# Performance work log

Measured on AMD Instinct MI355X. Metric: run time of the kernel, lower is better.

## Reference

```python
import jax, jax.numpy as jnp
import numpy as np

N = 8000      # nodes
E = 64000     # edges
F = 2560      # in_channels
H = 8         # heads
C = 320       # out_channels per head
G = 16        # graphs in batch
SLOPE = 0.2   # GATv2 default negative_slope


def setup_inputs() -> dict:
    key = jax.random.key(0)
    ks = jax.random.split(key, 20)
    inp = {
        'x': jax.random.normal(ks[0], (N, F), jnp.float32),
        'edge_index': jax.random.randint(ks[1], (2, E), 0, N, dtype=jnp.int64),
        'edge_attr': jax.random.normal(ks[2], (E, 1), jnp.float32),
        'batch': jnp.sort(jax.random.randint(ks[3], (N,), 0, G, dtype=jnp.int64)),
    }
    s_in = 1.0 / np.sqrt(F).astype(np.float32)
    s_att = 1.0 / np.sqrt(C).astype(np.float32)
    k = 4
    for layer in (1, 2):
        inp[f'Wl{layer}'] = jax.random.normal(ks[k + 0], (F, H * C), jnp.float32) * s_in
        inp[f'bl{layer}'] = jnp.zeros((H * C,), jnp.float32)
        inp[f'Wr{layer}'] = jax.random.normal(ks[k + 1], (F, H * C), jnp.float32) * s_in
        inp[f'br{layer}'] = jnp.zeros((H * C,), jnp.float32)
        inp[f'We{layer}'] = jax.random.normal(ks[k + 2], (1, H * C), jnp.float32)
        inp[f'att{layer}'] = jax.random.normal(ks[k + 3], (H, C), jnp.float32) * s_att
        inp[f'bias{layer}'] = jnp.zeros((H * C,), jnp.float32)
        k += 4
    return inp


def gatv2_layer(x, src, dst, edge_attr, Wl, bl, Wr, br, We, att, bias):
    # x: [N,F] -> out: [N, H*C]
    xl = (x @ Wl + bl).reshape(N, H, C)   # source transform (aggregated)
    xr = (x @ Wr + br).reshape(N, H, C)   # target transform
    ee = (edge_attr @ We).reshape(E, H, C)
    m = jax.nn.leaky_relu(xl[src] + xr[dst] + ee, SLOPE)  # [E,H,C]
    score = jnp.einsum('ehc,hc->eh', m, att)               # [E,H]
    # segment softmax over incoming edges of each target node
    smax = jax.ops.segment_max(score, dst, num_segments=N)  # [N,H]
    ex = jnp.exp(score - smax[dst])
    denom = jax.ops.segment_sum(ex, dst, num_segments=N)    # [N,H]
    alpha = ex / denom[dst]                                  # [E,H]
    out = jax.ops.segment_sum(xl[src] * alpha[:, :, None], dst, num_segments=N)
    return out.reshape(N, H * C) + bias


def reference(x, edge_index, edge_attr, batch,
              Wl1, bl1, Wr1, br1, We1, att1, bias1,
              Wl2, bl2, Wr2, br2, We2, att2, bias2):
    src, dst = edge_index[0], edge_index[1]
    h = gatv2_layer(x, src, dst, edge_attr, Wl1, bl1, Wr1, br1, We1, att1, bias1)
    # dropout is identity in eval mode
    h = gatv2_layer(h, src, dst, edge_attr, Wl2, bl2, Wr2, br2, We2, att2, bias2)
    # global mean pool over graphs
    sums = jax.ops.segment_sum(h, batch, num_segments=G)                 # [G, H*C]
    cnt = jax.ops.segment_sum(jnp.ones((N, 1), h.dtype), batch, num_segments=G)
    return sums / jnp.maximum(cnt, 1.0)
```

## Files before the change

kernel.cpp:

```cpp
#include <hip/hip_runtime.h>

typedef unsigned short u16;
typedef _Float16 f16;
typedef _Float16 f16x8 __attribute__((ext_vector_type(8)));
typedef float f32x4 __attribute__((ext_vector_type(4)));

#define AS1 __attribute__((address_space(1)))
#define AS3 __attribute__((address_space(3)))

constexpr int N_NODES = 8000;
constexpr int N_EDGES = 64000;
constexpr int F_IN    = 2560;
constexpr int HEADS   = 8;
constexpr int CPH     = 320;
constexpr int HC      = 2560;
constexpr int NW      = 5120;
constexpr int NGRAPH  = 16;
constexpr float SLOPE = 0.2f;

__global__ __launch_bounds__(256)
void cvt_f32_f16(const float* __restrict__ in, f16* __restrict__ out, int n)
{
  const int i = (blockIdx.x * 256 + threadIdx.x) * 4;
  if (i >= n) return;
  const float4 v = *(const float4*)(in + i);
  f16 o[4] = {(f16)v.x, (f16)v.y, (f16)v.z, (f16)v.w};
  *(ushort4*)(out + i) = *(const ushort4*)o;
}

__global__ __launch_bounds__(256)
void transpose_w(const float* __restrict__ in, f16* __restrict__ out)
{
  __shared__ u16 tile[64][66];
  const int bx = blockIdx.x * 64;
  const int by = blockIdx.y * 64;
  const int tx = threadIdx.x & 63;
  const int ty = threadIdx.x >> 6;
  #pragma unroll
  for (int i = ty; i < 64; i += 4) {
    f16 h = (f16)in[(size_t)(by + i) * HC + bx + tx];
    u16 u; __builtin_memcpy(&u, &h, 2);
    tile[i][tx] = u;
  }
  __syncthreads();
  #pragma unroll
  for (int i = ty; i < 64; i += 4) {
    u16 u = tile[tx][i];
    f16 h; __builtin_memcpy(&h, &u, 2);
    out[(size_t)(bx + i) * F_IN + by + tx] = h;
  }
}

__global__ __launch_bounds__(512)
void gemm_fused(const f16* __restrict__ A, const f16* __restrict__ BT,
                const float* __restrict__ bl, const float* __restrict__ br,
                f16* __restrict__ XL, f16* __restrict__ XR, int M)
{
  __shared__ __align__(16) f16 sA[256 * 32];
  __shared__ __align__(16) f16 sB[128 * 32];
  const int t    = threadIdx.x;
  const int lane = t & 63;
  const int wave = t >> 6;
  const int m0 = (blockIdx.x & 31) * 256;
  const int n0 = (blockIdx.x >> 5) * 128;
  const int fm = (wave >> 1) * 64;
  const int fn = (wave & 1) * 64;
  const int ml = lane & 15;
  const int lq = lane >> 4;

  f32x4 acc[4][4] = {};

  for (int k0 = 0; k0 < F_IN; k0 += 32) {
    __syncthreads();
    #pragma unroll
    for (int j = 0; j < 2; ++j) {
      const int s = j * 512 + t;
      const int r = s >> 2;
      const int lc = (s & 3) ^ ((r >> 1) & 3);
      int ra = m0 + r; ra = (ra < M) ? ra : (M - 1);
      const f16* ga = A + (size_t)ra * F_IN + k0 + lc * 8;
      __builtin_amdgcn_global_load_lds((AS1 const void*)ga,
                                       (AS3 void*)(sA + s * 8), 16, 0, 0);
    }
    {
      const int s = t;
      const int r = s >> 2;
      const int lc = (s & 3) ^ ((r >> 1) & 3);
      const f16* gb = BT + (size_t)(n0 + r) * F_IN + k0 + lc * 8;
      __builtin_amdgcn_global_load_lds((AS1 const void*)gb,
                                       (AS3 void*)(sB + s * 8), 16, 0, 0);
    }
    __syncthreads();

    f16x8 af[4], bfr[4];
    #pragma unroll
    for (int i = 0; i < 4; ++i) {
      const int row = fm + i * 16 + ml;
      const int p = lq ^ ((row >> 1) & 3);
      af[i] = *(const f16x8*)(sA + (row * 4 + p) * 8);
    }
    #pragma unroll
    for (int j = 0; j < 4; ++j) {
      const int row = fn + j * 16 + ml;
      const int p = lq ^ ((row >> 1) & 3);
      bfr[j] = *(const f16x8*)(sB + (row * 4 + p) * 8);
    }

    #pragma unroll
    for (int i = 0; i < 4; ++i)
      #pragma unroll
      for (int j = 0; j < 4; ++j)
        acc[i][j] = __builtin_amdgcn_mfma_f32_16x16x32_f16(af[i], bfr[j], acc[i][j], 0, 0, 0);
  }

  const bool left = (n0 < HC);
  f16* __restrict__ OUT = left ? XL : XR;
  const float* __restrict__ bias = left ? bl : br;
  const int nb = left ? n0 : (n0 - HC);
  const int rg = (lane >> 4) * 4;
  #pragma unroll
  for (int j = 0; j < 4; ++j) {
    const int gn = nb + fn + j * 16 + ml;
    const float bv = bias[gn];
    #pragma unroll
    for (int i = 0; i < 4; ++i) {
      #pragma unroll
      for (int r = 0; r < 4; ++r) {
        const int gm = m0 + fm + i * 16 + rg + r;
        if (gm < M) OUT[(size_t)gm * HC + gn] = (f16)(acc[i][j][r] + bv);
      }
    }
  }
}

__global__ __launch_bounds__(256)
void count_edges(const int* __restrict__ dst, int* __restrict__ counts)
{
  const int e = blockIdx.x * 256 + threadIdx.x;
  if (e < N_EDGES) atomicAdd(&counts[dst[e]], 1);
}

__global__ __launch_bounds__(256)
void scan_offsets(const int* __restrict__ counts, int* __restrict__ offs, int* __restrict__ cur)
{
  __shared__ int wtot[4];
  const int t = threadIdx.x;
  const int lane = t & 63, wave = t >> 6;
  const int base = t * 32;
  int loc[32];
  int run = 0;
  #pragma unroll
  for (int i = 0; i < 32; ++i) {
    const int idx = base + i;
    const int v = (idx < N_NODES) ? counts[idx] : 0;
    loc[i] = run;
    run += v;
  }
  int incl = run;
  #pragma unroll
  for (int off = 1; off < 64; off <<= 1) {
    int y = __shfl_up(incl, off, 64);
    if (lane >= off) incl += y;
  }
  const int excl = incl - run;
  if (lane == 63) wtot[wave] = incl;
  __syncthreads();
  int wb = 0;
  for (int wv = 0; wv < wave; ++wv) wb += wtot[wv];
  const int mybase = wb + excl;
  #pragma unroll
  for (int i = 0; i < 32; ++i) {
    const int idx = base + i;
    if (idx < N_NODES) { offs[idx] = mybase + loc[i]; cur[idx] = mybase + loc[i]; }
  }
  if (t == 255) offs[N_NODES] = wb + incl;
}

__global__ __launch_bounds__(256)
void fill_csr(const int* __restrict__ dst, int* __restrict__ cur, int* __restrict__ eids)
{
  const int e = blockIdx.x * 256 + threadIdx.x;
  if (e < N_EDGES) {
    const int p = atomicAdd(&cur[dst[e]], 1);
    eids[p] = e;
  }
}

__global__ __launch_bounds__(256)
void gat_edge_fused(const f16* __restrict__ XL, const f16* __restrict__ XR,
                    const float* __restrict__ We, const float* __restrict__ att,
                    const float* __restrict__ eattr,
                    const int* __restrict__ src,
                    const int* __restrict__ offs, const int* __restrict__ eids,
                    const float* __restrict__ bias,
                    f16* __restrict__ out)
{
  const int n    = blockIdx.x;
  const int t    = threadIdx.x;
  const int wave = t >> 6;
  const int lane = t & 63;
  const int half = lane >> 5;
  const int l32  = lane & 31;
  const int h    = wave * 2 + half;
  const int cb   = h * CPH + l32;

  float xr[10], wv[10], av[10];
  #pragma unroll
  for (int k = 0; k < 10; ++k) {
    const int c = cb + 32 * k;
    xr[k] = (float)XR[(size_t)n * HC + c];
    wv[k] = We[c];
    av[k] = att[c];
  }

  float m = -3.0e38f, l = 0.f;
  float acc[10];
  #pragma unroll
  for (int k = 0; k < 10; ++k) acc[k] = 0.f;

  const int b = offs[n], e = offs[n + 1];
  for (int p = b; p < e; ++p) {
    const int eid  = eids[p];
    const int s    = src[eid];
    const float ea = eattr[eid];
    const f16* row = XL + (size_t)s * HC;
    float xl[10];
    float partial = 0.f;
    #pragma unroll
    for (int k = 0; k < 10; ++k) {
      xl[k] = (float)row[cb + 32 * k];
      float v = xl[k] + xr[k] + ea * wv[k];
      v = (v > 0.f) ? v : SLOPE * v;
      partial += v * av[k];
    }
    #pragma unroll
    for (int msk = 16; msk >= 1; msk >>= 1)
      partial += __shfl_xor(partial, msk, 64);
    const float sc    = partial;
    const float mn    = fmaxf(m, sc);
    const float scale = __expf(m - mn);
    const float w     = __expf(sc - mn);
    l = l * scale + w;
    #pragma unroll
    for (int k = 0; k < 10; ++k) acc[k] = acc[k] * scale + w * xl[k];
    m = mn;
  }

  const float inv = (l > 0.f) ? 1.f / l : 0.f;
  #pragma unroll
  for (int k = 0; k < 10; ++k) {
    const int c = cb + 32 * k;
    out[(size_t)n * HC + c] = (f16)(acc[k] * inv + bias[c]);
  }
}

__global__ __launch_bounds__(256)
void pool_kernel(const f16* __restrict__ Hm, const int* __restrict__ batch, float* __restrict__ out)
{
  __shared__ int se[2];
  const int g = blockIdx.x;
  const int chunk = blockIdx.y;
  const int t = threadIdx.x;
  if (t < 2) {
    const int target = g + t;
    int lo = 0, hi = N_NODES;
    while (lo < hi) { const int mid = (lo + hi) >> 1; if (batch[mid] < target) lo = mid + 1; else hi = mid; }
    se[t] = lo;
  }
  __syncthreads();
  const int s0 = se[0], s1 = se[1];
  const int c = chunk * 256 + t;
  float sum = 0.f;
  for (int n = s0; n < s1; ++n) sum += (float)Hm[(size_t)n * HC + c];
  int cnt = s1 - s0; if (cnt < 1) cnt = 1;
  out[g * HC + c] = sum / (float)cnt;
}

static void run_layer(const f16* A, const float* Wl, const float* bl,
                      const float* Wr, const float* br,
                      const float* We, const float* att, const float* bias,
                      const int* src, const float* eattr,
                      f16* WT, f16* XL, f16* XR,
                      const int* offs, const int* eids, f16* OUT, hipStream_t stream)
{
  dim3 tgrid(HC / 64, F_IN / 64);
  transpose_w<<<tgrid, 256, 0, stream>>>(Wl, WT);
  transpose_w<<<tgrid, 256, 0, stream>>>(Wr, WT + (size_t)HC * F_IN);
  gemm_fused<<<32 * (NW / 128), 512, 0, stream>>>(A, WT, bl, br, XL, XR, N_NODES);
  gat_edge_fused<<<N_NODES, 256, 0, stream>>>(XL, XR, We, att, eattr, src, offs, eids, bias, OUT);
}

extern "C" void kernel_launch(void* const* d_in, const int* in_sizes, int n_in,
                              void* d_out, int out_size, void* d_ws, size_t ws_size,
                              hipStream_t stream)
{
  const float* x     = (const float*)d_in[0];
  const int*   eidx  = (const int*)d_in[1];
  const float* eattr = (const float*)d_in[2];
  const int*   batch = (const int*)d_in[3];
  const float* Wl1  = (const float*)d_in[4];
  const float* bl1  = (const float*)d_in[5];
  const float* Wr1  = (const float*)d_in[6];
  const float* br1  = (const float*)d_in[7];
  const float* We1  = (const float*)d_in[8];
  const float* att1 = (const float*)d_in[9];
  const float* bias1= (const float*)d_in[10];
  const float* Wl2  = (const float*)d_in[11];
  const float* bl2  = (const float*)d_in[12];
  const float* Wr2  = (const float*)d_in[13];
  const float* br2  = (const float*)d_in[14];
  const float* We2  = (const float*)d_in[15];
  const float* att2 = (const float*)d_in[16];
  const float* bias2= (const float*)d_in[17];
  float* out = (float*)d_out;

  const int* src = eidx;
  const int* dst = eidx + N_EDGES;

  char* w = (char*)d_ws;
  auto take = [&](size_t b) { char* p = w; w += (b + 255) & ~(size_t)255; return p; };
  f16*   Xh    = (f16*)take((size_t)N_NODES * F_IN * 2);
  f16*   H2h   = (f16*)take((size_t)N_NODES * HC * 2);
  f16*   WT    = (f16*)take((size_t)NW * F_IN * 2);
  f16*   XL    = (f16*)take((size_t)N_NODES * HC * 2);
  f16*   XR    = (f16*)take((size_t)N_NODES * HC * 2);
  int*   counts= (int*)take((size_t)N_NODES * 4);
  int*   offs  = (int*)take((size_t)(N_NODES + 1) * 4);
  int*   cur   = (int*)take((size_t)N_NODES * 4);
  int*   eids  = (int*)take((size_t)N_EDGES * 4);

  hipMemsetAsync(counts, 0, N_NODES * 4, stream);
  count_edges<<<N_EDGES / 256, 256, 0, stream>>>(dst, counts);
  scan_offsets<<<1, 256, 0, stream>>>(counts, offs, cur);
  fill_csr<<<N_EDGES / 256, 256, 0, stream>>>(dst, cur, eids);

  cvt_f32_f16<<<(N_NODES * F_IN) / 1024, 256, 0, stream>>>(x, Xh, N_NODES * F_IN);

  run_layer(Xh, Wl1, bl1, Wr1, br1, We1, att1, bias1, src, eattr,
            WT, XL, XR, offs, eids, Xh, stream);
  run_layer(Xh, Wl2, bl2, Wr2, br2, We2, att2, bias2, src, eattr,
            WT, XL, XR, offs, eids, H2h, stream);

  pool_kernel<<<dim3(NGRAPH, HC / 256), 256, 0, stream>>>(H2h, batch, out);
}
```

Measured before the change: 1.050 ms.

## Pipeline GEMM with double-buffered 256x256 tiles and vectorize edge kernel loads

The GEMM moves to 256x256 block tiles with K=64 stages, double-buffered in LDS (128KB), XOR-swizzled layouts, block-index remapping for L2 locality, and interleaved async global-to-LDS loads with MFMA phases using barriers and priority hints. The goal is to hide memory latency and raise data reuse in the dominant projection GEMM. Separately, the edge attention kernel switches to vectorized 16-byte and 4-byte loads and stores per lane, with a new channel mapping, to cut memory instruction count. The large LDS footprint and register pressure may reduce occupancy, and the hand-tuned waitcnt logic is fragile.

```diff
diff --git a/kernel.cpp b/kernel.cpp
--- a/kernel.cpp
+++ b/kernel.cpp
@@ -3,6 +3,7 @@
 typedef unsigned short u16;
 typedef _Float16 f16;
 typedef _Float16 f16x8 __attribute__((ext_vector_type(8)));
+typedef _Float16 f16x2 __attribute__((ext_vector_type(2)));
 typedef float f32x4 __attribute__((ext_vector_type(4)));
 
 #define AS1 __attribute__((address_space(1)))
@@ -51,67 +52,129 @@
   }
 }
 
-__global__ __launch_bounds__(512)
+__global__ __launch_bounds__(512, 2)
 void gemm_fused(const f16* __restrict__ A, const f16* __restrict__ BT,
                 const float* __restrict__ bl, const float* __restrict__ br,
-                f16* __restrict__ XL, f16* __restrict__ XR, int M)
-{
-  __shared__ __align__(16) f16 sA[256 * 32];
-  __shared__ __align__(16) f16 sB[128 * 32];
+                f16* __restrict__ XL, f16* __restrict__ XR)
+{
+  __shared__ __align__(16) f16 sm[65536];
+  f16* const sA0 = sm;
+  f16* const sA1 = sm + 16384;
+  f16* const sB0 = sm + 32768;
+  f16* const sB1 = sm + 49152;
+
   const int t    = threadIdx.x;
   const int lane = t & 63;
   const int wave = t >> 6;
-  const int m0 = (blockIdx.x & 31) * 256;
-  const int n0 = (blockIdx.x >> 5) * 128;
-  const int fm = (wave >> 1) * 64;
-  const int fn = (wave & 1) * 64;
+
+  int bid = (int)blockIdx.x;
+  bid = (bid & 7) * 80 + (bid >> 3);
+  const int m0 = (bid & 31) * 256;
+  const int n0 = (bid >> 5) * 256;
+
+  const int fm = (wave >> 2) * 128;
+  const int fn = (wave & 3) * 64;
   const int ml = lane & 15;
   const int lq = lane >> 4;
 
-  f32x4 acc[4][4] = {};
-
-  for (int k0 = 0; k0 < F_IN; k0 += 32) {
-    __syncthreads();
-    #pragma unroll
-    for (int j = 0; j < 2; ++j) {
-      const int s = j * 512 + t;
-      const int r = s >> 2;
-      const int lc = (s & 3) ^ ((r >> 1) & 3);
-      int ra = m0 + r; ra = (ra < M) ? ra : (M - 1);
-      const f16* ga = A + (size_t)ra * F_IN + k0 + lc * 8;
-      __builtin_amdgcn_global_load_lds((AS1 const void*)ga,
-                                       (AS3 void*)(sA + s * 8), 16, 0, 0);
+  auto stageA = [&](f16* D, int half, int kt) {
+    const int k0 = kt * 64;
+    #pragma unroll
+    for (int jj = 0; jj < 2; ++jj) {
+      const int s  = jj * 512 + t;
+      const int r  = s >> 3;
+      const int lc = (s & 7) ^ (r & 7);
+      int gr = m0 + half * 128 + r;
+      gr = (gr < N_NODES) ? gr : (N_NODES - 1);
+      const f16* g = A + (size_t)gr * F_IN + k0 + lc * 8;
+      __builtin_amdgcn_global_load_lds((AS1 const void*)g,
+                                       (AS3 void*)(D + half * 8192 + s * 8), 16, 0, 0);
     }
-    {
-      const int s = t;
-      const int r = s >> 2;
-      const int lc = (s & 3) ^ ((r >> 1) & 3);
-      const f16* gb = BT + (size_t)(n0 + r) * F_IN + k0 + lc * 8;
-      __builtin_amdgcn_global_load_lds((AS1 const void*)gb,
-                                       (AS3 void*)(sB + s * 8), 16, 0, 0);
+  };
+  auto stageB = [&](f16* D, int half, int kt) {
+    const int k0 = kt * 64;
+    #pragma unroll
+    for (int jj = 0; jj < 2; ++jj) {
+      const int s  = jj * 512 + t;
+      const int r  = s >> 3;
+      const int lc = (s & 7) ^ (r & 7);
+      const f16* g = BT + (size_t)(n0 + half * 128 + r) * F_IN + k0 + lc * 8;
+      __builtin_amdgcn_global_load_lds((AS1 const void*)g,
+                                       (AS3 void*)(D + half * 8192 + s * 8), 16, 0, 0);
     }
-    __syncthreads();
-
-    f16x8 af[4], bfr[4];
-    #pragma unroll
-    for (int i = 0; i < 4; ++i) {
-      const int row = fm + i * 16 + ml;
-      const int p = lq ^ ((row >> 1) & 3);
-      af[i] = *(const f16x8*)(sA + (row * 4 + p) * 8);
+  };
+  auto ldA = [&](const f16* S, int i, int kk) -> f16x8 {
+    const int row = fm + i * 16 + ml;
+    const int p   = (kk * 4 + lq) ^ (row & 7);
+    return *(const f16x8*)(S + row * 64 + p * 8);
+  };
+  auto ldB = [&](const f16* S, int j, int kk) -> f16x8 {
+    const int row = fn + j * 16 + ml;
+    const int p   = (kk * 4 + lq) ^ (row & 7);
+    return *(const f16x8*)(S + row * 64 + p * 8);
+  };
+
+  f32x4 acc[8][4] = {};
+  f16x8 bf[4][2];
+
+#define MMROW(i, A0_, A1_)                                                                   \
+    _Pragma("unroll")                                                                        \
+    for (int j = 0; j < 4; ++j) {                                                            \
+      acc[i][j] = __builtin_amdgcn_mfma_f32_16x16x32_f16(A0_, bf[j][0], acc[i][j], 0, 0, 0); \
+      acc[i][j] = __builtin_amdgcn_mfma_f32_16x16x32_f16(A1_, bf[j][1], acc[i][j], 0, 0, 0); \
     }
-    #pragma unroll
-    for (int j = 0; j < 4; ++j) {
-      const int row = fn + j * 16 + ml;
-      const int p = lq ^ ((row >> 1) & 3);
-      bfr[j] = *(const f16x8*)(sB + (row * 4 + p) * 8);
-    }
-
-    #pragma unroll
-    for (int i = 0; i < 4; ++i)
-      #pragma unroll
-      for (int j = 0; j < 4; ++j)
-        acc[i][j] = __builtin_amdgcn_mfma_f32_16x16x32_f16(af[i], bfr[j], acc[i][j], 0, 0, 0);
-  }
+
+#define PHASE(SA, q, STG)                          \
+  {                                                \
+    const f16x8 p00 = ldA(SA, 2*(q),     0);       \
+    const f16x8 p01 = ldA(SA, 2*(q),     1);       \
+    const f16x8 p10 = ldA(SA, 2*(q) + 1, 0);       \
+    const f16x8 p11 = ldA(SA, 2*(q) + 1, 1);       \
+    STG;                                           \
+    __builtin_amdgcn_s_barrier();                  \
+    __builtin_amdgcn_sched_barrier(0);             \
+    __builtin_amdgcn_s_setprio(1);                 \
+    MMROW(2*(q),     p00, p01)                     \
+    MMROW(2*(q) + 1, p10, p11)                     \
+    __builtin_amdgcn_s_setprio(0);                 \
+  }
+
+#define ENDPH() { __builtin_amdgcn_s_barrier(); __builtin_amdgcn_sched_barrier(0); }
+#define LOADB(SB) { _Pragma("unroll") for (int j = 0; j < 4; ++j) { bf[j][0] = ldB(SB, j, 0); bf[j][1] = ldB(SB, j, 1); } }
+
+  stageA(sA0, 0, 0); stageA(sA0, 1, 0);
+  stageB(sB0, 0, 0); stageB(sB0, 1, 0);
+  stageB(sB1, 0, 1); stageB(sB1, 1, 1);
+  asm volatile("s_waitcnt vmcnt(4)" ::: "memory");
+  __builtin_amdgcn_s_barrier();
+  __builtin_amdgcn_sched_barrier(0);
+
+  for (int it = 0; it < 20; ++it) {
+    const int T  = 2 * it;
+    const int t1 = T + 1;
+    const int t2 = (T + 2 < 40) ? T + 2 : 39;
+    const int t3 = (T + 3 < 40) ? T + 3 : 39;
+
+    LOADB(sB0)
+    PHASE(sA0, 0, stageA(sA1, 0, t1)) ENDPH()
+    PHASE(sA0, 1, stageA(sA1, 1, t1)) ENDPH()
+    PHASE(sA0, 2, stageB(sB0, 0, t2)) ENDPH()
+    PHASE(sA0, 3, stageB(sB0, 1, t2))
+    asm volatile("s_waitcnt vmcnt(4)" ::: "memory");
+    ENDPH()
+    LOADB(sB1)
+    PHASE(sA1, 0, stageA(sA0, 0, t2)) ENDPH()
+    PHASE(sA1, 1, stageA(sA0, 1, t2)) ENDPH()
+    PHASE(sA1, 2, stageB(sB1, 0, t3)) ENDPH()
+    PHASE(sA1, 3, stageB(sB1, 1, t3))
+    asm volatile("s_waitcnt vmcnt(4)" ::: "memory");
+    ENDPH()
+  }
+
+#undef MMROW
+#undef PHASE
+#undef ENDPH
+#undef LOADB
 
   const bool left = (n0 < HC);
   f16* __restrict__ OUT = left ? XL : XR;
@@ -123,11 +186,11 @@
     const int gn = nb + fn + j * 16 + ml;
     const float bv = bias[gn];
     #pragma unroll
-    for (int i = 0; i < 4; ++i) {
+    for (int i = 0; i < 8; ++i) {
       #pragma unroll
       for (int r = 0; r < 4; ++r) {
         const int gm = m0 + fm + i * 16 + rg + r;
-        if (gm < M) OUT[(size_t)gm * HC + gn] = (f16)(acc[i][j][r] + bv);
+        if (gm < N_NODES) OUT[(size_t)gm * HC + gn] = (f16)(acc[i][j][r] + bv);
       }
     }
   }
@@ -202,15 +265,28 @@
   const int half = lane >> 5;
   const int l32  = lane & 31;
   const int h    = wave * 2 + half;
-  const int cb   = h * CPH + l32;
+  const int c8   = h * CPH + l32 * 8;
+  const int c2   = h * CPH + 256 + l32 * 2;
 
   float xr[10], wv[10], av[10];
-  #pragma unroll
-  for (int k = 0; k < 10; ++k) {
-    const int c = cb + 32 * k;
-    xr[k] = (float)XR[(size_t)n * HC + c];
-    wv[k] = We[c];
-    av[k] = att[c];
+  {
+    const f16x8 v8 = *(const f16x8*)(XR + (size_t)n * HC + c8);
+    const f16x2 v2 = *(const f16x2*)(XR + (size_t)n * HC + c2);
+    #pragma unroll
+    for (int k = 0; k < 8; ++k) xr[k] = (float)v8[k];
+    xr[8] = (float)v2[0]; xr[9] = (float)v2[1];
+  }
+  {
+    const float4 w0 = *(const float4*)(We + c8);
+    const float4 w1 = *(const float4*)(We + c8 + 4);
+    const float4 a0 = *(const float4*)(att + c8);
+    const float4 a1 = *(const float4*)(att + c8 + 4);
+    wv[0]=w0.x; wv[1]=w0.y; wv[2]=w0.z; wv[3]=w0.w;
+    wv[4]=w1.x; wv[5]=w1.y; wv[6]=w1.z; wv[7]=w1.w;
+    av[0]=a0.x; av[1]=a0.y; av[2]=a0.z; av[3]=a0.w;
+    av[4]=a1.x; av[5]=a1.y; av[6]=a1.z; av[7]=a1.w;
+    wv[8] = We[c2]; wv[9] = We[c2 + 1];
+    av[8] = att[c2]; av[9] = att[c2 + 1];
   }
 
   float m = -3.0e38f, l = 0.f;
@@ -224,11 +300,15 @@
     const int s    = src[eid];
     const float ea = eattr[eid];
     const f16* row = XL + (size_t)s * HC;
+    const f16x8 v8 = *(const f16x8*)(row + c8);
+    const f16x2 v2 = *(const f16x2*)(row + c2);
     float xl[10];
+    #pragma unroll
+    for (int k = 0; k < 8; ++k) xl[k] = (float)v8[k];
+    xl[8] = (float)v2[0]; xl[9] = (float)v2[1];
     float partial = 0.f;
     #pragma unroll
     for (int k = 0; k < 10; ++k) {
-      xl[k] = (float)row[cb + 32 * k];
       float v = xl[k] + xr[k] + ea * wv[k];
       v = (v > 0.f) ? v : SLOPE * v;
       partial += v * av[k];
@@ -247,11 +327,14 @@
   }
 
   const float inv = (l > 0.f) ? 1.f / l : 0.f;
-  #pragma unroll
-  for (int k = 0; k < 10; ++k) {
-    const int c = cb + 32 * k;
-    out[(size_t)n * HC + c] = (f16)(acc[k] * inv + bias[c]);
-  }
+  f16x8 s8;
+  #pragma unroll
+  for (int k = 0; k < 8; ++k) s8[k] = (f16)(acc[k] * inv + bias[c8 + k]);
+  f16x2 s2;
+  s2[0] = (f16)(acc[8] * inv + bias[c2]);
+  s2[1] = (f16)(acc[9] * inv + bias[c2 + 1]);
+  *(f16x8*)(out + (size_t)n * HC + c8) = s8;
+  *(f16x2*)(out + (size_t)n * HC + c2) = s2;
 }
 
 __global__ __launch_bounds__(256)
@@ -286,7 +369,7 @@
   dim3 tgrid(HC / 64, F_IN / 64);
   transpose_w<<<tgrid, 256, 0, stream>>>(Wl, WT);
   transpose_w<<<tgrid, 256, 0, stream>>>(Wr, WT + (size_t)HC * F_IN);
-  gemm_fused<<<32 * (NW / 128), 512, 0, stream>>>(A, WT, bl, br, XL, XR, N_NODES);
+  gemm_fused<<<32 * (NW / 256), 512, 0, stream>>>(A, WT, bl, br, XL, XR);
   gat_edge_fused<<<N_NODES, 256, 0, stream>>>(XL, XR, We, att, eattr, src, offs, eids, bias, OUT);
 }
 
```

New measurement: 1.010 ms. 3.8% less time.
